# Kernel optimization log

Measured on AMD Instinct MI355X. Metric: run time of the kernel, lower is better.

The kernel has to match this reference:

```python
import jax, jax.numpy as jnp
import numpy as np

DIM_Q = 1024
DIM_KV = 768
N_HEADS = 4


def setup_inputs() -> dict:
    key = jax.random.key(0)
    ks = jax.random.split(key, 7)
    b, lq, lkv = 4, 2048, 2048
    q = jax.random.normal(ks[0], (b, lq, DIM_Q), dtype=jnp.float32)
    kv = jax.random.normal(ks[1], (b, lkv, DIM_KV), dtype=jnp.float32)
    s_q = 1.0 / np.sqrt(DIM_Q)
    s_kv = 1.0 / np.sqrt(DIM_KV)
    Wq = jax.random.normal(ks[2], (DIM_Q, DIM_Q), dtype=jnp.float32) * s_q
    Wk = jax.random.normal(ks[3], (DIM_Q, DIM_KV), dtype=jnp.float32) * s_kv
    Wv = jax.random.normal(ks[4], (DIM_Q, DIM_KV), dtype=jnp.float32) * s_kv
    Wo = jax.random.normal(ks[5], (DIM_Q, DIM_Q), dtype=jnp.float32) * s_q
    bo = jax.random.normal(ks[6], (DIM_Q,), dtype=jnp.float32) * 0.01
    return {"q": q, "kv": kv, "Wq": Wq, "Wk": Wk, "Wv": Wv, "Wo": Wo, "bo": bo}


def _split_heads(x):
    # [b, l, d] -> [b, h, l, d/h]
    b, l, d = x.shape
    return x.reshape(b, l, N_HEADS, d // N_HEADS).transpose(0, 2, 1, 3)


def reference(q, kv, Wq, Wk, Wv, Wo, bo):
    qp = q @ Wq.T               # [b, lq, dim_q]
    kp = kv @ Wk.T              # [b, lkv, dim_q]
    vp = kv @ Wv.T              # [b, lkv, dim_q]
    qh, kh, vh = _split_heads(qp), _split_heads(kp), _split_heads(vp)
    scale = (DIM_Q // N_HEADS) ** (-0.5)
    scores = jnp.einsum('bhqd,bhkd->bhqk', qh, kh) * scale
    attn = jax.nn.softmax(scores, axis=-1)
    ctx = jnp.einsum('bhqk,bhkd->bhqd', attn, vh)  # [b, h, lq, hd]
    b, h, lq, hd = ctx.shape
    ctx = ctx.transpose(0, 2, 1, 3).reshape(b, lq, h * hd)
    return ctx @ Wo.T + bo
```

## Files before the change

### kernel.cpp

```cpp
#include <hip/hip_runtime.h>

#define DIMQ 1024
#define NH 4
#define HD 256
#define BSZ 4
#define LQ 2048
#define LKV 2048
#define KVN 2048

typedef __attribute__((ext_vector_type(8))) short bf16x8;
typedef __attribute__((ext_vector_type(4))) float f32x4;

__device__ inline unsigned short f32_to_bf16(float f) {
  union { float f; unsigned u; } v; v.f = f;
  unsigned u = v.u;
  return (unsigned short)((u + 0x7fffu + ((u >> 16) & 1u)) >> 16);
}

__device__ inline uint4 ld8cvt(const float* p, float scale) {
  const float4 a = *(const float4*)p;
  const float4 b = *(const float4*)(p + 4);
  union { unsigned short s[8]; uint4 v; } r;
  r.s[0] = f32_to_bf16(a.x * scale); r.s[1] = f32_to_bf16(a.y * scale);
  r.s[2] = f32_to_bf16(a.z * scale); r.s[3] = f32_to_bf16(a.w * scale);
  r.s[4] = f32_to_bf16(b.x * scale); r.s[5] = f32_to_bf16(b.y * scale);
  r.s[6] = f32_to_bf16(b.z * scale); r.s[7] = f32_to_bf16(b.w * scale);
  return r.v;
}

__device__ __forceinline__ void gl2lds16(const void* gptr, void* lptr) {
  __builtin_amdgcn_global_load_lds(
      (const __attribute__((address_space(1))) void*)gptr,
      (__attribute__((address_space(3))) void*)lptr, 16, 0, 0);
}

__global__ __launch_bounds__(256)
void cvt5(const float* s0, const float* s1, const float* s2, const float* s3,
          const float* s4, unsigned short* d0, unsigned short* d1,
          unsigned short* d2, unsigned short* d3, unsigned short* d4,
          long n0, long n1, long n2, long n3, long n4,
          float c0, float c1, float c2, float c3, float c4) {
  const float* s; unsigned short* d; long n; float c;
  switch (blockIdx.y) {
    case 0: s = s0; d = d0; n = n0; c = c0; break;
    case 1: s = s1; d = d1; n = n1; c = c1; break;
    case 2: s = s2; d = d2; n = n2; c = c2; break;
    case 3: s = s3; d = d3; n = n3; c = c3; break;
    default: s = s4; d = d4; n = n4; c = c4; break;
  }
  long i = ((long)blockIdx.x * 256 + threadIdx.x) * 8;
  if (i < n) *(uint4*)(d + i) = ld8cvt(s + i, c);
}

__global__ __launch_bounds__(256)
void transpose_k(const unsigned short* __restrict__ vp,
                 unsigned short* __restrict__ vpT,
                 int src_stride, int src_off) {
  __shared__ unsigned short T[64][64];
  const int l0g = blockIdx.x * 64;
  const int b = l0g / LKV, l0 = l0g % LKV;
  const int n0 = blockIdx.y * 64;
  const int tid = threadIdx.x;
  const int r = tid >> 3, c = tid & 7;
#pragma unroll
  for (int p = 0; p < 2; ++p) {
    int row = p * 32 + r;
    *(uint4*)&T[row][(c ^ ((row >> 3) & 7)) * 8] =
        *(const uint4*)(vp + (size_t)(l0g + row) * src_stride + src_off + n0 + c * 8);
  }
  __syncthreads();
#pragma unroll
  for (int p = 0; p < 2; ++p) {
    int n = p * 32 + r;
    union { unsigned short s[8]; uint4 v; } t;
#pragma unroll
    for (int j = 0; j < 8; ++j) {
      int row = c * 8 + j;
      t.s[j] = T[row][(((n >> 3) ^ ((row >> 3) & 7)) << 3) | (n & 7)];
    }
    *(uint4*)(vpT + ((size_t)b * DIMQ + n0 + n) * LKV + l0 + c * 8) = t.v;
  }
}

template<typename TOUT, bool HAS_BIAS>
__global__ __launch_bounds__(256)
void gemm_bt(const unsigned short* __restrict__ A,
             const unsigned short* __restrict__ Bm,
             const float* __restrict__ bias,
             TOUT* __restrict__ C,
             int M, int N, int K) {
  __shared__ alignas(16) unsigned short As[128 * 64];
  __shared__ alignas(16) unsigned short Bs[128 * 64];
  const int tid = threadIdx.x;
  const int lane = tid & 63;
  const int wave = tid >> 6;
  const int wr = (wave >> 1) * 64, wc = (wave & 1) * 64;
  const int l15 = lane & 15, quad = lane >> 4;
  const int srow = lane >> 3, scol = lane & 7;
  const int m0 = blockIdx.x * 128;
  const int n0 = blockIdx.y * 128;

  f32x4 acc[4][4] = {};
  for (int k0 = 0; k0 < K; k0 += 64) {
    __syncthreads();
#pragma unroll
    for (int i = 0; i < 4; ++i) {
      int c = wave * 4 + i;
      gl2lds16(A + (size_t)(m0 + c * 8 + srow) * K + k0 + scol * 8, As + c * 512);
      gl2lds16(Bm + (size_t)(n0 + c * 8 + srow) * K + k0 + scol * 8, Bs + c * 512);
    }
    __syncthreads();
#pragma unroll
    for (int kh = 0; kh < 2; ++kh) {
      bf16x8 af[4], bfr[4];
#pragma unroll
      for (int i = 0; i < 4; ++i)
        af[i] = *(const bf16x8*)(As + (wr + i * 16 + l15) * 64 + kh * 32 + quad * 8);
#pragma unroll
      for (int j = 0; j < 4; ++j)
        bfr[j] = *(const bf16x8*)(Bs + (wc + j * 16 + l15) * 64 + kh * 32 + quad * 8);
#pragma unroll
      for (int i = 0; i < 4; ++i)
#pragma unroll
        for (int j = 0; j < 4; ++j)
          acc[i][j] = __builtin_amdgcn_mfma_f32_16x16x32_bf16(af[i], bfr[j], acc[i][j], 0, 0, 0);
    }
  }

#pragma unroll
  for (int j = 0; j < 4; ++j) {
    int n = n0 + wc + j * 16 + l15;
    float bv = 0.f;
    if (HAS_BIAS) bv = bias[n];
#pragma unroll
    for (int i = 0; i < 4; ++i) {
      int mb = m0 + wr + i * 16 + quad * 4;
#pragma unroll
      for (int r = 0; r < 4; ++r) {
        float v = acc[i][j][r] + bv;
        if constexpr (sizeof(TOUT) == 2)
          C[(size_t)(mb + r) * N + n] = f32_to_bf16(v);
        else
          C[(size_t)(mb + r) * N + n] = v;
      }
    }
  }
}

__global__ __launch_bounds__(256, 2)
void attn(const unsigned short* __restrict__ qp,
          const unsigned short* __restrict__ kpv,
          const unsigned short* __restrict__ vpT,
          unsigned short* __restrict__ ctx) {
  __shared__ alignas(16) unsigned short Ks[64 * 256];
  __shared__ alignas(16) unsigned short Vt[256 * 64];
  __shared__ alignas(16) unsigned short Ps[64 * 64];
  __shared__ float Ls[64][2];
  const int tid = threadIdx.x, lane = tid & 63, wave = tid >> 6;
  const int l15 = lane & 15, quad = lane >> 4;
  const int qh = wave >> 1;
  const int kvh = wave & 1;
  const int b = blockIdx.z, h = blockIdx.y;
  const int q0 = blockIdx.x * 64;
  const size_t base = (size_t)b * LQ * DIMQ + h * HD;

  bf16x8 qf[2][8];
#pragma unroll
  for (int im = 0; im < 2; ++im) {
    const unsigned short* qrow =
        qp + base + (size_t)(q0 + qh * 32 + im * 16 + l15) * DIMQ;
#pragma unroll
    for (int s = 0; s < 8; ++s)
      qf[im][s] = *(const bf16x8*)(qrow + s * 32 + quad * 8);
  }

  f32x4 oacc[2][8] = {};
  float lrow[2][4] = {};

  const unsigned short* kb = kpv + (size_t)b * LKV * KVN + h * HD;
  const unsigned short* vtb = vpT + ((size_t)b * DIMQ + h * HD) * LKV;

  const int krow_l = lane >> 5;
  const int kcol_l = lane & 31;
  const int vrow_l = lane >> 3;
  const int vcol_l = lane & 7;

#pragma unroll
  for (int i = 0; i < 8; ++i) {
    int c = i * 4 + wave;
    int row = 2 * c + krow_l;
    gl2lds16(kb + (size_t)row * KVN + ((kcol_l ^ (row & 7)) << 3), Ks + c * 512);
  }
  __syncthreads();

  for (int kv0 = 0; kv0 < LKV; kv0 += 64) {
#pragma unroll
    for (int i = 0; i < 8; ++i) {
      int c = i * 4 + wave;
      int row = 8 * c + vrow_l;
      gl2lds16(vtb + (size_t)row * LKV + kv0 + ((vcol_l ^ (row & 7)) << 3),
               Vt + c * 512);
    }

    f32x4 sacc[2][2] = {};
    const int r0 = kvh * 32 + l15, r1 = r0 + 16;
#pragma unroll
    for (int s = 0; s < 8; ++s) {
      bf16x8 kf0 = *(const bf16x8*)(Ks + r0 * 256 + (((s * 4 + quad) ^ (r0 & 7)) << 3));
      bf16x8 kf1 = *(const bf16x8*)(Ks + r1 * 256 + (((s * 4 + quad) ^ (r1 & 7)) << 3));
      sacc[0][0] = __builtin_amdgcn_mfma_f32_16x16x32_bf16(qf[0][s], kf0, sacc[0][0], 0, 0, 0);
      sacc[0][1] = __builtin_amdgcn_mfma_f32_16x16x32_bf16(qf[0][s], kf1, sacc[0][1], 0, 0, 0);
      sacc[1][0] = __builtin_amdgcn_mfma_f32_16x16x32_bf16(qf[1][s], kf0, sacc[1][0], 0, 0, 0);
      sacc[1][1] = __builtin_amdgcn_mfma_f32_16x16x32_bf16(qf[1][s], kf1, sacc[1][1], 0, 0, 0);
    }

    const int c0 = kvh * 32 + l15, c1 = c0 + 16;
#pragma unroll
    for (int im = 0; im < 2; ++im)
#pragma unroll
      for (int i = 0; i < 4; ++i) {
        int row = qh * 32 + im * 16 + quad * 4 + i;
        float p0 = __expf(sacc[im][0][i]);
        float p1 = __expf(sacc[im][1][i]);
        Ps[row * 64 + ((((c0 >> 3) ^ (row & 7)) << 3) | (c0 & 7))] = f32_to_bf16(p0);
        Ps[row * 64 + ((((c1 >> 3) ^ (row & 7)) << 3) | (c1 & 7))] = f32_to_bf16(p1);
        lrow[im][i] += p0 + p1;
      }
    __syncthreads();

    if (kv0 + 64 < LKV) {
#pragma unroll
      for (int i = 0; i < 8; ++i) {
        int c = i * 4 + wave;
        int row = 2 * c + krow_l;
        gl2lds16(kb + (size_t)(kv0 + 64 + row) * KVN + ((kcol_l ^ (row & 7)) << 3),
                 Ks + c * 512);
      }
    }

    const int pr0 = qh * 32 + l15, pr1 = pr0 + 16;
#pragma unroll
    for (int u = 0; u < 2; ++u) {
      bf16x8 pf0 = *(const bf16x8*)(Ps + pr0 * 64 + (((u * 4 + quad) ^ (pr0 & 7)) << 3));
      bf16x8 pf1 = *(const bf16x8*)(Ps + pr1 * 64 + (((u * 4 + quad) ^ (pr1 & 7)) << 3));
#pragma unroll
      for (int jn = 0; jn < 8; ++jn) {
        int vr = kvh * 128 + jn * 16 + l15;
        bf16x8 vf = *(const bf16x8*)(Vt + vr * 64 + (((u * 4 + quad) ^ (vr & 7)) << 3));
        oacc[0][jn] = __builtin_amdgcn_mfma_f32_16x16x32_bf16(pf0, vf, oacc[0][jn], 0, 0, 0);
        oacc[1][jn] = __builtin_amdgcn_mfma_f32_16x16x32_bf16(pf1, vf, oacc[1][jn], 0, 0, 0);
      }
    }
    __syncthreads();
  }

#pragma unroll
  for (int im = 0; im < 2; ++im)
#pragma unroll
    for (int i = 0; i < 4; ++i) {
      float l = lrow[im][i];
      l += __shfl_xor(l, 1);
      l += __shfl_xor(l, 2);
      l += __shfl_xor(l, 4);
      l += __shfl_xor(l, 8);
      if (l15 == 0) Ls[qh * 32 + im * 16 + quad * 4 + i][kvh] = l;
    }
  __syncthreads();

  unsigned short* cb = ctx + base;
#pragma unroll
  for (int im = 0; im < 2; ++im)
#pragma unroll
    for (int r = 0; r < 4; ++r) {
      int row = qh * 32 + im * 16 + quad * 4 + r;
      float inv = 1.0f / (Ls[row][0] + Ls[row][1]);
#pragma unroll
      for (int jn = 0; jn < 8; ++jn) {
        int col = kvh * 128 + jn * 16 + l15;
        cb[(size_t)(q0 + row) * DIMQ + col] = f32_to_bf16(oacc[im][jn][r] * inv);
      }
    }
}

extern "C" void kernel_launch(void* const* d_in, const int* in_sizes, int n_in,
                              void* d_out, int out_size, void* d_ws, size_t ws_size,
                              hipStream_t stream) {
  const float* q  = (const float*)d_in[0];
  const float* kv = (const float*)d_in[1];
  const float* Wq = (const float*)d_in[2];
  const float* Wk = (const float*)d_in[3];
  const float* Wv = (const float*)d_in[4];
  const float* Wo = (const float*)d_in[5];
  const float* bo = (const float*)d_in[6];
  float* out = (float*)d_out;

  const long NQ = (long)BSZ * LQ * DIMQ;
  const long NKV = (long)BSZ * LKV * 768;
  const long NWQ = (long)DIMQ * DIMQ;
  const long NWK = (long)DIMQ * 768;

  unsigned short* q_bf = (unsigned short*)d_out;
  unsigned short* kpv  = (unsigned short*)d_out;
  unsigned short* kv_bf = (unsigned short*)d_ws;
  unsigned short* ctx   = kv_bf;
  unsigned short* Wq_bf = kv_bf + NQ;
  unsigned short* Wk_bf = Wq_bf + NWQ;
  unsigned short* Wv_bf = Wk_bf + NWK;
  unsigned short* Wo_bf = Wv_bf + NWK;
  unsigned short* qp    = Wo_bf + NWQ;
  unsigned short* vpT   = qp + NQ;

  dim3 blk(256);
  const int M = BSZ * LQ;

  cvt5<<<dim3(3072, 5), blk, 0, stream>>>(kv, Wq, Wk, Wv, Wo,
                                          kv_bf, Wq_bf, Wk_bf, Wv_bf, Wo_bf,
                                          NKV, NWQ, NWK, NWK, NWQ,
                                          1.0f, 0.0625f, 1.0f, 1.0f, 1.0f);
  cvt5<<<dim3(4096, 1), blk, 0, stream>>>(q, nullptr, nullptr, nullptr, nullptr,
                                          q_bf, nullptr, nullptr, nullptr, nullptr,
                                          NQ, 0, 0, 0, 0,
                                          1.0f, 0.f, 0.f, 0.f, 0.f);
  gemm_bt<unsigned short, false><<<dim3(M/128, DIMQ/128), blk, 0, stream>>>(q_bf, Wq_bf, nullptr, qp, M, DIMQ, 1024);
  gemm_bt<unsigned short, false><<<dim3(M/128, KVN/128), blk, 0, stream>>>(kv_bf, Wk_bf, nullptr, kpv, M, KVN, 768);
  transpose_k<<<dim3(M/64, DIMQ/64), blk, 0, stream>>>(kpv, vpT, KVN, 1024);
  attn<<<dim3(LQ/64, NH, BSZ), blk, 0, stream>>>(qp, kpv, vpT, ctx);
  gemm_bt<float, true><<<dim3(M/128, DIMQ/128), blk, 0, stream>>>(ctx, Wo_bf, bo, out, M, DIMQ, 1024);
}
```

Measured before the change: 308.4 us.

## Merge conversion launches, fold log2e into Wq, pack P stores, add MFMA priority

The two fp32-to-bf16 conversion launches are merged into a single six-way kernel. The log2(e) factor is folded into the Wq scaling so softmax can use exp2f instead of __expf. K rows are loaded into LDS in a permuted order so each lane's two adjacent score columns are written to P as one packed 32-bit store instead of two 16-bit stores. s_setprio is raised around the MFMA loops to favour matrix issue across waves. Together these aim to cut launch overhead, exp cost and LDS write traffic, at the cost of more intricate index mapping that must stay consistent between the K loads and the P layout.

```diff
diff --git a/kernel.cpp b/kernel.cpp
--- a/kernel.cpp
+++ b/kernel.cpp
@@ -35,18 +35,20 @@
 }
 
 __global__ __launch_bounds__(256)
-void cvt5(const float* s0, const float* s1, const float* s2, const float* s3,
-          const float* s4, unsigned short* d0, unsigned short* d1,
-          unsigned short* d2, unsigned short* d3, unsigned short* d4,
-          long n0, long n1, long n2, long n3, long n4,
-          float c0, float c1, float c2, float c3, float c4) {
+void cvt6(const float* s0, const float* s1, const float* s2, const float* s3,
+          const float* s4, const float* s5,
+          unsigned short* d0, unsigned short* d1, unsigned short* d2,
+          unsigned short* d3, unsigned short* d4, unsigned short* d5,
+          long n0, long n1, long n2, long n3, long n4, long n5,
+          float c0, float c1, float c2, float c3, float c4, float c5) {
   const float* s; unsigned short* d; long n; float c;
   switch (blockIdx.y) {
     case 0: s = s0; d = d0; n = n0; c = c0; break;
     case 1: s = s1; d = d1; n = n1; c = c1; break;
     case 2: s = s2; d = d2; n = n2; c = c2; break;
     case 3: s = s3; d = d3; n = n3; c = c3; break;
-    default: s = s4; d = d4; n = n4; c = c4; break;
+    case 4: s = s4; d = d4; n = n4; c = c4; break;
+    default: s = s5; d = d5; n = n5; c = c5; break;
   }
   long i = ((long)blockIdx.x * 256 + threadIdx.x) * 8;
   if (i < n) *(uint4*)(d + i) = ld8cvt(s + i, c);
@@ -189,7 +191,8 @@
   for (int i = 0; i < 8; ++i) {
     int c = i * 4 + wave;
     int row = 2 * c + krow_l;
-    gl2lds16(kb + (size_t)row * KVN + ((kcol_l ^ (row & 7)) << 3), Ks + c * 512);
+    int lr = (row & 32) + ((row & 15) << 1) + ((row >> 4) & 1);
+    gl2lds16(kb + (size_t)lr * KVN + ((kcol_l ^ (row & 7)) << 3), Ks + c * 512);
   }
   __syncthreads();
 
@@ -204,6 +207,7 @@
 
     f32x4 sacc[2][2] = {};
     const int r0 = kvh * 32 + l15, r1 = r0 + 16;
+    __builtin_amdgcn_s_setprio(1);
 #pragma unroll
     for (int s = 0; s < 8; ++s) {
       bf16x8 kf0 = *(const bf16x8*)(Ks + r0 * 256 + (((s * 4 + quad) ^ (r0 & 7)) << 3));
@@ -213,17 +217,19 @@
       sacc[1][0] = __builtin_amdgcn_mfma_f32_16x16x32_bf16(qf[1][s], kf0, sacc[1][0], 0, 0, 0);
       sacc[1][1] = __builtin_amdgcn_mfma_f32_16x16x32_bf16(qf[1][s], kf1, sacc[1][1], 0, 0, 0);
     }
-
-    const int c0 = kvh * 32 + l15, c1 = c0 + 16;
+    __builtin_amdgcn_s_setprio(0);
+
+    const int dw = kvh * 16 + l15;
+    const int t16 = dw >> 2, sub = dw & 3;
 #pragma unroll
     for (int im = 0; im < 2; ++im)
 #pragma unroll
       for (int i = 0; i < 4; ++i) {
         int row = qh * 32 + im * 16 + quad * 4 + i;
-        float p0 = __expf(sacc[im][0][i]);
-        float p1 = __expf(sacc[im][1][i]);
-        Ps[row * 64 + ((((c0 >> 3) ^ (row & 7)) << 3) | (c0 & 7))] = f32_to_bf16(p0);
-        Ps[row * 64 + ((((c1 >> 3) ^ (row & 7)) << 3) | (c1 & 7))] = f32_to_bf16(p1);
+        float p0 = exp2f(sacc[im][0][i]);
+        float p1 = exp2f(sacc[im][1][i]);
+        unsigned pw = (unsigned)f32_to_bf16(p0) | ((unsigned)f32_to_bf16(p1) << 16);
+        *(unsigned*)(Ps + row * 64 + (((t16 ^ (row & 7)) << 3) | (sub * 2))) = pw;
         lrow[im][i] += p0 + p1;
       }
     __syncthreads();
@@ -233,12 +239,14 @@
       for (int i = 0; i < 8; ++i) {
         int c = i * 4 + wave;
         int row = 2 * c + krow_l;
-        gl2lds16(kb + (size_t)(kv0 + 64 + row) * KVN + ((kcol_l ^ (row & 7)) << 3),
+        int lr = (row & 32) + ((row & 15) << 1) + ((row >> 4) & 1);
+        gl2lds16(kb + (size_t)(kv0 + 64 + lr) * KVN + ((kcol_l ^ (row & 7)) << 3),
                  Ks + c * 512);
       }
     }
 
     const int pr0 = qh * 32 + l15, pr1 = pr0 + 16;
+    __builtin_amdgcn_s_setprio(1);
 #pragma unroll
     for (int u = 0; u < 2; ++u) {
       bf16x8 pf0 = *(const bf16x8*)(Ps + pr0 * 64 + (((u * 4 + quad) ^ (pr0 & 7)) << 3));
@@ -251,6 +259,7 @@
         oacc[1][jn] = __builtin_amdgcn_mfma_f32_16x16x32_bf16(pf1, vf, oacc[1][jn], 0, 0, 0);
       }
     }
+    __builtin_amdgcn_s_setprio(0);
     __syncthreads();
   }
 
@@ -313,14 +322,11 @@
   dim3 blk(256);
   const int M = BSZ * LQ;
 
-  cvt5<<<dim3(3072, 5), blk, 0, stream>>>(kv, Wq, Wk, Wv, Wo,
-                                          kv_bf, Wq_bf, Wk_bf, Wv_bf, Wo_bf,
-                                          NKV, NWQ, NWK, NWK, NWQ,
-                                          1.0f, 0.0625f, 1.0f, 1.0f, 1.0f);
-  cvt5<<<dim3(4096, 1), blk, 0, stream>>>(q, nullptr, nullptr, nullptr, nullptr,
-                                          q_bf, nullptr, nullptr, nullptr, nullptr,
-                                          NQ, 0, 0, 0, 0,
-                                          1.0f, 0.f, 0.f, 0.f, 0.f);
+  cvt6<<<dim3(4096, 6), blk, 0, stream>>>(
+      kv, Wq, Wk, Wv, Wo, q,
+      kv_bf, Wq_bf, Wk_bf, Wv_bf, Wo_bf, q_bf,
+      NKV, NWQ, NWK, NWK, NWQ, NQ,
+      1.0f, 0.0625f * 1.44269504088896f, 1.0f, 1.0f, 1.0f, 1.0f);
   gemm_bt<unsigned short, false><<<dim3(M/128, DIMQ/128), blk, 0, stream>>>(q_bf, Wq_bf, nullptr, qp, M, DIMQ, 1024);
   gemm_bt<unsigned short, false><<<dim3(M/128, KVN/128), blk, 0, stream>>>(kv_bf, Wk_bf, nullptr, kpv, M, KVN, 768);
   transpose_k<<<dim3(M/64, DIMQ/64), blk, 0, stream>>>(kpv, vpT, KVN, 1024);
```

Result: no change. 307.5 us (-0.3%).
